# Kernel optimization log

Hardware: AMD Instinct MI355X
Metric: run time of the kernel (lower is better)

Reference implementation:

```python
import jax, jax.numpy as jnp
import numpy as np

V, D, HID, HEADS = 50000, 128, 128, 4
N, E, G = 100000, 1600000, 256
CH = HID // HEADS  # per-head channels for layer 1


def setup_inputs() -> dict:
    key = jax.random.key(0)
    ks = jax.random.split(key, 16)
    g = lambda i, shape, scale=0.05: jax.random.normal(ks[i], shape, jnp.float32) * scale
    return {
        "x_lex": jax.random.randint(ks[0], (N,), 0, V),
        "edge_index": jax.random.randint(ks[1], (2, E), 0, N),
        "batch": jnp.sort(jax.random.randint(ks[2], (N,), 0, G)),
        "emb": g(3, (V, D)),
        "W1": g(4, (D, HID)), "a1_src": g(5, (HEADS, CH)), "a1_dst": g(6, (HEADS, CH)), "b1": jnp.zeros((HID,), jnp.float32),
        "W2": g(7, (HID, HID)), "a2_src": g(8, (1, HID)), "a2_dst": g(9, (1, HID)), "b2": jnp.zeros((HID,), jnp.float32),
        "Wc1": g(10, (HID, HID // 2)), "bc1": jnp.zeros((HID // 2,), jnp.float32),
        "Wc2": g(11, (HID // 2, 1)), "bc2": jnp.zeros((1,), jnp.float32),
    }


def gat_layer(x, src, dst, W, a_src, a_dst, b, heads, ch):
    """PyG-style GATConv (v1), concat=True, negative_slope=0.2."""
    n = x.shape[0]
    h = (x @ W).reshape(n, heads, ch)                 # [N,H,C]
    al_s = (h * a_src).sum(-1)                        # [N,H]
    al_d = (h * a_dst).sum(-1)                        # [N,H]
    e = jax.nn.leaky_relu(al_s[src] + al_d[dst], 0.2) # [Etot,H]
    # segment softmax over incoming edges per destination node
    m = jax.ops.segment_max(e, dst, num_segments=n)
    ex = jnp.exp(e - m[dst])
    s = jax.ops.segment_sum(ex, dst, num_segments=n)
    alpha = ex / s[dst]
    out = jax.ops.segment_sum(alpha[:, :, None] * h[src], dst, num_segments=n)  # [N,H,C]
    return out.reshape(n, heads * ch) + b


def reference(x_lex, edge_index, batch, emb, W1, a1_src, a1_dst, b1, W2, a2_src, a2_dst, b2, Wc1, bc1, Wc2, bc2):
    n = x_lex.shape[0]
    loops = jnp.arange(n)  # GATConv adds self-loops by default
    src = jnp.concatenate([edge_index[0], loops])
    dst = jnp.concatenate([edge_index[1], loops])
    x = emb[x_lex]                                               # [N,D]
    h = jax.nn.elu(gat_layer(x, src, dst, W1, a1_src, a1_dst, b1, HEADS, CH))
    h = jax.nn.elu(gat_layer(h, src, dst, W2, a2_src, a2_dst, b2, 1, HID))
    sums = jax.ops.segment_sum(h, batch, num_segments=G)
    cnt = jax.ops.segment_sum(jnp.ones((n,), h.dtype), batch, num_segments=G)
    h_pool = sums / jnp.maximum(cnt, 1.0)[:, None]               # global mean pool [G,HID]
    logits = jax.nn.relu(h_pool @ Wc1 + bc1) @ Wc2 + bc2         # [G,1]
    return (logits, h_pool)
```

## Files before the change

kernel.cpp:

```cpp
#include <hip/hip_runtime.h>
#include <hip/hip_bf16.h>
#include <math.h>

#define P_CHUNK 8192
#define NBKT 1024
#define CAP  4096

typedef float f4 __attribute__((ext_vector_type(4)));

__device__ __forceinline__ float lrelu(float x){ return x < 0.f ? 0.2f*x : x; }
__device__ __forceinline__ float elu_(float x){ return x > 0.f ? x : expm1f(x); }


template<int H, bool GATHER>
__device__ __forceinline__ void gemm_body(float (*xs)[132], int bid,
    const float* __restrict__ X, const int* __restrict__ idx,
    const float* __restrict__ W, const float* __restrict__ asrc,
    const float* __restrict__ adst, float* __restrict__ Hout,
    float* __restrict__ als, float* __restrict__ ald, int n)
{
  int tid = threadIdx.x;
  int tr = tid >> 5, tc = tid & 31;
  int r8 = tr*8, c4 = tc*4;
  int row0 = bid * 64;

  #pragma unroll
  for (int j=0;j<8;j++){
    int e = tid + j*256;
    int r = e >> 5, cq = e & 31;
    int gr = row0 + r;
    f4 v = (f4)(0.f);
    if (gr < n){
      int srow = GATHER ? idx[gr] : gr;
      v = *reinterpret_cast<const f4*>(&X[(size_t)srow*128 + cq*4]);
    }
    *reinterpret_cast<f4*>(&xs[r][cq*4]) = v;
  }
  __syncthreads();

  float acc[8][4];
  #pragma unroll
  for (int r=0;r<8;r++)
    #pragma unroll
    for (int i=0;i<4;i++) acc[r][i] = 0.f;

  #pragma unroll 4
  for (int kq=0;kq<32;kq++){
    int k0 = kq*4;
    f4 xv[8], wv[4];
    #pragma unroll
    for (int i=0;i<8;i++) xv[i] = *reinterpret_cast<const f4*>(&xs[r8+i][k0]);
    #pragma unroll
    for (int kk=0;kk<4;kk++) wv[kk] = *reinterpret_cast<const f4*>(&W[(size_t)(k0+kk)*128 + c4]);
    #pragma unroll
    for (int kk=0;kk<4;kk++)
      #pragma unroll
      for (int i=0;i<8;i++)
        #pragma unroll
        for (int j=0;j<4;j++)
          acc[i][j] = fmaf(xv[i][kk], wv[kk][j], acc[i][j]);
  }

  const f4 asv = *reinterpret_cast<const f4*>(&asrc[c4]);
  const f4 adv = *reinterpret_cast<const f4*>(&adst[c4]);
  const int GT = 32 / H;
  int hh = tc / GT;

  #pragma unroll
  for (int r=0;r<8;r++){
    int gr = row0 + r8 + r;
    if (gr < n){
      f4 o = { acc[r][0], acc[r][1], acc[r][2], acc[r][3] };
      *reinterpret_cast<f4*>(&Hout[(size_t)gr*128 + c4]) = o;
    }
    float ps = acc[r][0]*asv[0] + acc[r][1]*asv[1] + acc[r][2]*asv[2] + acc[r][3]*asv[3];
    float pd = acc[r][0]*adv[0] + acc[r][1]*adv[1] + acc[r][2]*adv[2] + acc[r][3]*adv[3];
    #pragma unroll
    for (int m=1;m<GT;m<<=1){ ps += __shfl_xor(ps,m); pd += __shfl_xor(pd,m); }
    if ((tc & (GT-1)) == 0 && gr < n){
      als[(size_t)gr*H + hh] = ps;
      ald[(size_t)gr*H + hh] = pd;
    }
  }
}

__device__ __forceinline__ void p3_body(int* lh, int bid,
    const int* __restrict__ ei, int E, int Etot,
    int* __restrict__ bcur, int* __restrict__ tmp)
{
  int* lbase = lh + NBKT;
  int tid = threadIdx.x;
  for (int t = tid; t < NBKT; t += 256) lh[t] = 0;
  __syncthreads();
  int base = bid * P_CHUNK;
  for (int j = 0; j < P_CHUNK; j += 256){
    int i = base + j + tid;
    if (i < Etot){
      int dst = (i < E) ? ei[E + i] : (i - E);
      atomicAdd(&lh[dst >> 7], 1);
    }
  }
  __syncthreads();
  for (int t = tid; t < NBKT; t += 256){
    int v = lh[t];
    lbase[t] = v ? atomicAdd(&bcur[t], v) : 0;
  }
  __syncthreads();
  for (int t = tid; t < NBKT; t += 256) lh[t] = 0;
  __syncthreads();
  for (int j = 0; j < P_CHUNK; j += 256){
    int i = base + j + tid;
    if (i < Etot){
      int s, d;
      if (i < E){ s = ei[i]; d = ei[E + i]; } else { s = i - E; d = i - E; }
      int b = d >> 7;
      int r = atomicAdd(&lh[b], 1);
      tmp[b*CAP + lbase[b] + r] = s | ((d & 127) << 17);
    }
  }
}

__global__ __launch_bounds__(256) void k_gemm1_p3(
    const float* __restrict__ X, const int* __restrict__ idx,
    const float* __restrict__ W, const float* __restrict__ asrc,
    const float* __restrict__ adst, float* __restrict__ Hout,
    float* __restrict__ als, float* __restrict__ ald, int n, int gb,
    const int* __restrict__ ei, int E, int Etot,
    int* __restrict__ bcur, int* __restrict__ tmp)
{
  __shared__ __align__(16) char smem[64*132*4];
  if ((int)blockIdx.x < gb){
    gemm_body<4,true>(reinterpret_cast<float(*)[132]>(smem), blockIdx.x,
                      X, idx, W, asrc, adst, Hout, als, ald, n);
  } else {
    p3_body(reinterpret_cast<int*>(smem), blockIdx.x - gb, ei, E, Etot, bcur, tmp);
  }
}

template<int H, bool GATHER>
__global__ __launch_bounds__(256) void gemm_al(
    const float* __restrict__ X, const int* __restrict__ idx,
    const float* __restrict__ W, const float* __restrict__ asrc,
    const float* __restrict__ adst, float* __restrict__ Hout,
    float* __restrict__ als, float* __restrict__ ald, int n)
{
  __shared__ float xs[64][132];
  gemm_body<H,GATHER>(xs, blockIdx.x, X, idx, W, asrc, adst, Hout, als, ald, n);
}

__global__ __launch_bounds__(256) void p4local(const int* __restrict__ tmp,
                                               const int* __restrict__ bcnt,
                                               int* __restrict__ off, int* __restrict__ srcs,
                                               int N, int Etot){
  __shared__ int cnt[128];
  __shared__ int offL[128];
  __shared__ int wred[4];
  __shared__ int e0sh;
  int b = blockIdx.x, tid = threadIdx.x, lane = tid & 63, w = tid >> 6;

  int partial = 0;
  for (int t = tid; t < b; t += 256) partial += bcnt[t];
  #pragma unroll
  for (int sh=1; sh<64; sh<<=1) partial += __shfl_xor(partial, sh);
  if (lane == 0) wred[w] = partial;
  if (tid < 128) cnt[tid] = 0;
  __syncthreads();
  if (tid == 0){
    e0sh = wred[0] + wred[1] + wred[2] + wred[3];
    if (b == 0) off[N] = Etot;
  }
  __syncthreads();
  int e0 = e0sh;
  int ne = bcnt[b];
  const int* slab = tmp + (size_t)b*CAP;

  for (int j = tid; j < ne; j += 256)
    atomicAdd(&cnt[(slab[j] >> 17) & 127], 1);
  __syncthreads();
  if (tid < 64){
    int v0 = cnt[2*tid], v1 = cnt[2*tid + 1];
    int p = v0 + v1;
    int x = p;
    #pragma unroll
    for (int d = 1; d < 64; d <<= 1){ int y = __shfl_up(x, d); if (tid >= d) x += y; }
    int excl = x - p;
    offL[2*tid]     = excl;
    offL[2*tid + 1] = excl + v0;
  }
  __syncthreads();
  if (tid < 128){
    int gd = b*128 + tid;
    if (gd < N) off[gd] = e0 + offL[tid];
    cnt[tid] = 0;
  }
  __syncthreads();
  for (int j = tid; j < ne; j += 256){
    int e = slab[j];
    int d = (e >> 17) & 127;
    int r = atomicAdd(&cnt[d], 1);
    srcs[e0 + offL[d] + r] = e & 0x1FFFF;
  }
}

template<int H>
__global__ __launch_bounds__(256) void aggr(
    const float* __restrict__ h, const float* __restrict__ als,
    const float* __restrict__ ald, const int* __restrict__ srcs,
    const int* __restrict__ off, const float* __restrict__ bias,
    float* __restrict__ out, int n)
{
  __shared__ float s_p[4][64*H];
  __shared__ int   s_s[4][64];
  int tid = threadIdx.x;
  int wid = tid >> 6, lane = tid & 63;
  int d = blockIdx.x*4 + wid;
  if (d >= n) return;
  int half = lane >> 5, ch = lane & 31;
  int c4 = ch*4;
  const int hh = (H==1) ? 0 : (ch >> 3);

  int s0 = off[d], s1 = off[d+1];

  float adv[H];
  #pragma unroll
  for (int q=0;q<H;q++) adv[q] = ald[(size_t)d*H + q];

  float m[H], ssum[H];
  #pragma unroll
  for (int q=0;q<H;q++){ m[q] = -INFINITY; ssum[q] = 0.f; }
  float a0=0.f, a1=0.f, a2=0.f, a3=0.f;

  for (int base = s0; base < s1; base += 64){
    int cl = s1 - base; if (cl > 64) cl = 64;

    int sv = 0;
    float e[H];
    if (lane < cl){
      sv = srcs[base + lane];
      #pragma unroll
      for (int q=0;q<H;q++) e[q] = lrelu(als[(size_t)sv*H + q] + adv[q]);
    } else {
      #pragma unroll
      for (int q=0;q<H;q++) e[q] = -INFINITY;
    }

    float cm[H];
    #pragma unroll
    for (int q=0;q<H;q++) cm[q] = e[q];
    #pragma unroll
    for (int sh=1; sh<64; sh<<=1){
      #pragma unroll
      for (int q=0;q<H;q++) cm[q] = fmaxf(cm[q], __shfl_xor(cm[q], sh));
    }

    float p[H], sc[H];
    #pragma unroll
    for (int q=0;q<H;q++){
      float nm = fmaxf(m[q], cm[q]);
      sc[q] = __expf(m[q] - nm);
      ssum[q] *= sc[q];
      m[q] = nm;
      p[q] = __expf(e[q] - nm);
    }
    float schh = sc[0];
    #pragma unroll
    for (int q=1;q<H;q++) schh = (hh==q) ? sc[q] : schh;
    a0 *= schh; a1 *= schh; a2 *= schh; a3 *= schh;

    float cs[H];
    #pragma unroll
    for (int q=0;q<H;q++) cs[q] = p[q];
    #pragma unroll
    for (int sh=1; sh<64; sh<<=1){
      #pragma unroll
      for (int q=0;q<H;q++) cs[q] += __shfl_xor(cs[q], sh);
    }
    #pragma unroll
    for (int q=0;q<H;q++) ssum[q] += cs[q];

    #pragma unroll
    for (int q=0;q<H;q++) s_p[wid][lane*H + q] = p[q];
    s_s[wid][lane] = sv;

    for (int j = half; j < cl; j += 2){
      int s = s_s[wid][j];
      float w = s_p[wid][j*H + hh];
      const float4 hv = *reinterpret_cast<const float4*>(&h[(size_t)s*128 + c4]);
      a0 = fmaf(w, hv.x, a0);
      a1 = fmaf(w, hv.y, a1);
      a2 = fmaf(w, hv.z, a2);
      a3 = fmaf(w, hv.w, a3);
    }
  }

  a0 += __shfl_xor(a0, 32);
  a1 += __shfl_xor(a1, 32);
  a2 += __shfl_xor(a2, 32);
  a3 += __shfl_xor(a3, 32);

  float den = ssum[0];
  #pragma unroll
  for (int q=1;q<H;q++) den = (hh==q) ? ssum[q] : den;
  float inv = 1.f / den;

  if (half == 0){
    const float4 bv = *reinterpret_cast<const float4*>(&bias[c4]);
    float4 o;
    o.x = elu_(a0*inv + bv.x);
    o.y = elu_(a1*inv + bv.y);
    o.z = elu_(a2*inv + bv.z);
    o.w = elu_(a3*inv + bv.w);
    *reinterpret_cast<float4*>(&out[(size_t)d*128 + c4]) = o;
  }
}

__global__ __launch_bounds__(256) void kpool(const float* __restrict__ act,
    const int* __restrict__ batch, int n, float* __restrict__ pool)
{
  __shared__ int sb[2];
  __shared__ float part[128];
  int g = blockIdx.x, tid = threadIdx.x;
  if (tid == 0){
    int lo=0, hi=n;
    while (lo<hi){ int mid=(lo+hi)>>1; if (batch[mid] < g) lo=mid+1; else hi=mid; }
    sb[0]=lo;
    int lo2=lo, hi2=n;
    while (lo2<hi2){ int mid=(lo2+hi2)>>1; if (batch[mid] < g+1) lo2=mid+1; else hi2=mid; }
    sb[1]=lo2;
  }
  __syncthreads();
  int lo=sb[0], hi=sb[1];
  int c = tid & 127, half = tid >> 7;
  float acc = 0.f;
  for (int i=lo+half; i<hi; i+=2) acc += act[(size_t)i*128 + c];
  if (half == 0) part[c] = acc;
  __syncthreads();
  if (half == 1) part[c] += acc;
  __syncthreads();
  if (half == 0){
    float cnt = (float)(hi-lo);
    pool[(size_t)g*128 + c] = part[c] / fmaxf(cnt, 1.f);
  }
}

__global__ __launch_bounds__(64) void kclassify(const float* __restrict__ pool,
    const float* __restrict__ Wc1, const float* __restrict__ bc1,
    const float* __restrict__ Wc2, const float* __restrict__ bc2,
    float* __restrict__ logits)
{
  int g = blockIdx.x, j = threadIdx.x;
  const float* hp = pool + (size_t)g*128;
  float t = bc1[j];
  #pragma unroll 8
  for (int c=0;c<128;c++) t = fmaf(hp[c], Wc1[c*64+j], t);
  t = fmaxf(t, 0.f) * Wc2[j];
  for (int m=1;m<64;m<<=1) t += __shfl_xor(t, m);
  if (j==0) logits[g] = t + bc2[0];
}

extern "C" void kernel_launch(void* const* d_in, const int* in_sizes, int n_in,
                              void* d_out, int out_size, void* d_ws, size_t ws_size,
                              hipStream_t stream)
{
  const int*   x_lex = (const int*)d_in[0];
  const int*   ei    = (const int*)d_in[1];
  const int*   batch = (const int*)d_in[2];
  const float* emb   = (const float*)d_in[3];
  const float* W1    = (const float*)d_in[4];
  const float* a1s   = (const float*)d_in[5];
  const float* a1d   = (const float*)d_in[6];
  const float* b1    = (const float*)d_in[7];
  const float* W2    = (const float*)d_in[8];
  const float* a2s   = (const float*)d_in[9];
  const float* a2d   = (const float*)d_in[10];
  const float* b2    = (const float*)d_in[11];
  const float* Wc1   = (const float*)d_in[12];
  const float* bc1   = (const float*)d_in[13];
  const float* Wc2   = (const float*)d_in[14];
  const float* bc2   = (const float*)d_in[15];

  int N = in_sizes[0];
  int E = in_sizes[1] / 2;
  int Etot = E + N;
  const int G = 256;

  char* p = (char*)d_ws;
  float* hbuf   = (float*)p;          p += (size_t)N*128*4;
  float* act    = (float*)p;          p += (size_t)N*128*4;
  float* als    = (float*)p;          p += (size_t)N*4*4;
  float* ald    = (float*)p;          p += (size_t)N*4*4;
  int*   off    = (int*)p;            p += (size_t)(N+1)*4;
  int*   srcs   = (int*)p;            p += (size_t)Etot*4;
  int*   bcur   = (int*)p;
  int*   tmp    = (int*)act;

  hipMemsetAsync(bcur, 0, NBKT*4, stream);
  int nblk = (Etot + P_CHUNK - 1) / P_CHUNK;
  int nb   = (N + 127) / 128;
  int gb   = (N + 63) / 64;
  k_gemm1_p3<<<gb + nblk, 256, 0, stream>>>(emb, x_lex, W1, a1s, a1d, hbuf, als, ald, N, gb,
                                            ei, E, Etot, bcur, tmp);
  p4local<<<nb, 256, 0, stream>>>(tmp, bcur, off, srcs, N, Etot);

  aggr<4><<<(N+3)/4,256,0,stream>>>(hbuf, als, ald, srcs, off, b1, act, N);

  gemm_al<1,false><<<gb,256,0,stream>>>(act, nullptr, W2, a2s, a2d, hbuf, als, ald, N);
  aggr<1><<<(N+3)/4,256,0,stream>>>(hbuf, als, ald, srcs, off, b2, act, N);

  float* out = (float*)d_out;
  kpool<<<G,256,0,stream>>>(act, batch, N, out + G);
  kclassify<<<G,64,0,stream>>>(out + G, Wc1, bc1, Wc2, bc2, out);
}
```

Measured before the change: 484.6 us.

## Enlarge GEMM tile to 128 rows with 8x8 register blocking per thread

The fused gather-GEMM computing attention logits now processes 128 rows per block, and each thread accumulates an 8x8 output tile instead of 8x4. This halves the block count and raises the number of FMAs per W load and LDS read, cutting global and shared-memory traffic per output. The cost is doubled shared memory (about 67KB), which also grows the fused p3 blocks, plus more registers, so occupancy may drop. A small unroll hint is also added to the edge-aggregation inner loop.

```diff
diff --git a/kernel.cpp b/kernel.cpp
--- a/kernel.cpp
+++ b/kernel.cpp
@@ -20,12 +20,12 @@
     float* __restrict__ als, float* __restrict__ ald, int n)
 {
   int tid = threadIdx.x;
-  int tr = tid >> 5, tc = tid & 31;
-  int r8 = tr*8, c4 = tc*4;
-  int row0 = bid * 64;
-
-  #pragma unroll
-  for (int j=0;j<8;j++){
+  int tr = tid >> 4, tc = tid & 15;
+  int r8 = tr*8, c8 = tc*8;
+  int row0 = bid * 128;
+
+  #pragma unroll
+  for (int j=0;j<16;j++){
     int e = tid + j*256;
     int r = e >> 5, cq = e & 31;
     int gr = row0 + r;
@@ -38,43 +38,55 @@
   }
   __syncthreads();
 
-  float acc[8][4];
+  float acc[8][8];
   #pragma unroll
   for (int r=0;r<8;r++)
     #pragma unroll
-    for (int i=0;i<4;i++) acc[r][i] = 0.f;
-
-  #pragma unroll 4
+    for (int i=0;i<8;i++) acc[r][i] = 0.f;
+
+  #pragma unroll 2
   for (int kq=0;kq<32;kq++){
     int k0 = kq*4;
-    f4 xv[8], wv[4];
+    f4 xv[8], wv0[4], wv1[4];
     #pragma unroll
     for (int i=0;i<8;i++) xv[i] = *reinterpret_cast<const f4*>(&xs[r8+i][k0]);
     #pragma unroll
-    for (int kk=0;kk<4;kk++) wv[kk] = *reinterpret_cast<const f4*>(&W[(size_t)(k0+kk)*128 + c4]);
+    for (int kk=0;kk<4;kk++){
+      wv0[kk] = *reinterpret_cast<const f4*>(&W[(size_t)(k0+kk)*128 + c8]);
+      wv1[kk] = *reinterpret_cast<const f4*>(&W[(size_t)(k0+kk)*128 + c8 + 4]);
+    }
     #pragma unroll
     for (int kk=0;kk<4;kk++)
       #pragma unroll
-      for (int i=0;i<8;i++)
+      for (int i=0;i<8;i++){
         #pragma unroll
-        for (int j=0;j<4;j++)
-          acc[i][j] = fmaf(xv[i][kk], wv[kk][j], acc[i][j]);
-  }
-
-  const f4 asv = *reinterpret_cast<const f4*>(&asrc[c4]);
-  const f4 adv = *reinterpret_cast<const f4*>(&adst[c4]);
-  const int GT = 32 / H;
+        for (int j=0;j<4;j++){
+          acc[i][j]   = fmaf(xv[i][kk], wv0[kk][j], acc[i][j]);
+          acc[i][j+4] = fmaf(xv[i][kk], wv1[kk][j], acc[i][j+4]);
+        }
+      }
+  }
+
+  const f4 as0 = *reinterpret_cast<const f4*>(&asrc[c8]);
+  const f4 as1 = *reinterpret_cast<const f4*>(&asrc[c8+4]);
+  const f4 ad0 = *reinterpret_cast<const f4*>(&adst[c8]);
+  const f4 ad1 = *reinterpret_cast<const f4*>(&adst[c8+4]);
+  const int GT = 16 / H;
   int hh = tc / GT;
 
   #pragma unroll
   for (int r=0;r<8;r++){
     int gr = row0 + r8 + r;
     if (gr < n){
-      f4 o = { acc[r][0], acc[r][1], acc[r][2], acc[r][3] };
-      *reinterpret_cast<f4*>(&Hout[(size_t)gr*128 + c4]) = o;
-    }
-    float ps = acc[r][0]*asv[0] + acc[r][1]*asv[1] + acc[r][2]*asv[2] + acc[r][3]*asv[3];
-    float pd = acc[r][0]*adv[0] + acc[r][1]*adv[1] + acc[r][2]*adv[2] + acc[r][3]*adv[3];
+      f4 o0 = { acc[r][0], acc[r][1], acc[r][2], acc[r][3] };
+      f4 o1 = { acc[r][4], acc[r][5], acc[r][6], acc[r][7] };
+      *reinterpret_cast<f4*>(&Hout[(size_t)gr*128 + c8])     = o0;
+      *reinterpret_cast<f4*>(&Hout[(size_t)gr*128 + c8 + 4]) = o1;
+    }
+    float ps = acc[r][0]*as0[0] + acc[r][1]*as0[1] + acc[r][2]*as0[2] + acc[r][3]*as0[3]
+             + acc[r][4]*as1[0] + acc[r][5]*as1[1] + acc[r][6]*as1[2] + acc[r][7]*as1[3];
+    float pd = acc[r][0]*ad0[0] + acc[r][1]*ad0[1] + acc[r][2]*ad0[2] + acc[r][3]*ad0[3]
+             + acc[r][4]*ad1[0] + acc[r][5]*ad1[1] + acc[r][6]*ad1[2] + acc[r][7]*ad1[3];
     #pragma unroll
     for (int m=1;m<GT;m<<=1){ ps += __shfl_xor(ps,m); pd += __shfl_xor(pd,m); }
     if ((tc & (GT-1)) == 0 && gr < n){
@@ -128,7 +140,7 @@
     const int* __restrict__ ei, int E, int Etot,
     int* __restrict__ bcur, int* __restrict__ tmp)
 {
-  __shared__ __align__(16) char smem[64*132*4];
+  __shared__ __align__(16) char smem[128*132*4];
   if ((int)blockIdx.x < gb){
     gemm_body<4,true>(reinterpret_cast<float(*)[132]>(smem), blockIdx.x,
                       X, idx, W, asrc, adst, Hout, als, ald, n);
@@ -144,7 +156,7 @@
     const float* __restrict__ adst, float* __restrict__ Hout,
     float* __restrict__ als, float* __restrict__ ald, int n)
 {
-  __shared__ float xs[64][132];
+  __shared__ float xs[128][132];
   gemm_body<H,GATHER>(xs, blockIdx.x, X, idx, W, asrc, adst, Hout, als, ald, n);
 }
 
@@ -282,6 +294,7 @@
     for (int q=0;q<H;q++) s_p[wid][lane*H + q] = p[q];
     s_s[wid][lane] = sv;
 
+    #pragma unroll 2
     for (int j = half; j < cl; j += 2){
       int s = s_s[wid][j];
       float w = s_p[wid][j*H + hh];
@@ -397,7 +410,7 @@
   hipMemsetAsync(bcur, 0, NBKT*4, stream);
   int nblk = (Etot + P_CHUNK - 1) / P_CHUNK;
   int nb   = (N + 127) / 128;
-  int gb   = (N + 63) / 64;
+  int gb   = (N + 127) / 128;
   k_gemm1_p3<<<gb + nblk, 256, 0, stream>>>(emb, x_lex, W1, a1s, a1d, hbuf, als, ald, N, gb,
                                             ei, E, Etot, bcur, tmp);
   p4local<<<nb, 256, 0, stream>>>(tmp, bcur, off, srcs, N, Etot);
```

After: 486.9 us. About the same (+0.5%).
